# Kernel optimization log

Hardware: AMD Instinct MI355X
Metric: run time of the kernel (lower is better)

The kernel has to match this reference:

```python
import jax, jax.numpy as jnp
import numpy as np

N = 100000      # nodes per graph
E = 1600000     # edges (avg degree 16)
T = 4           # time steps
NL = 15         # num_locations
FD = 3          # feature_dim_node
H, C = 2, 6     # heads, per-head channels (hidden_channels=12)
HC = H * C


def setup_inputs():
    key = jax.random.key(0)
    ks = jax.random.split(key, 24)
    inp = {
        'node_types': jax.random.randint(ks[0], (T, N), 0, 4, dtype=jnp.int32),
        'requests': jax.random.normal(ks[1], (T, N), jnp.float32),
        'time_index': jax.random.uniform(ks[2], (T, N), dtype=jnp.float32),
        'edge_index': jax.random.randint(ks[3], (T, 2, E), 0, N, dtype=jnp.int32),
        'emb': 0.1 * jax.random.normal(ks[4], (4, FD), jnp.float32),
    }
    dims = [FD + 2, HC, HC, HC]
    k = 5
    for i, din in enumerate(dims):
        inp[f'W{i}'] = jax.random.normal(ks[k], (din, HC), jnp.float32) / np.sqrt(din); k += 1
        inp[f'as{i}'] = 0.1 * jax.random.normal(ks[k], (H, C), jnp.float32); k += 1
        inp[f'ad{i}'] = 0.1 * jax.random.normal(ks[k], (H, C), jnp.float32); k += 1
        inp[f'b{i}'] = jnp.zeros((HC,), jnp.float32); k += 1
    return inp


def gat_layer(x, src, dst, W, a_s, a_d, b):
    # PyG GATConv: linear -> per-head additive attention -> softmax over incoming
    # edges (self-loops already appended to src/dst) -> weighted aggregation.
    h = (x @ W).reshape(N, H, C)
    e_s = (h * a_s).sum(-1)                                  # [N, H]
    e_d = (h * a_d).sum(-1)                                  # [N, H]
    logits = jax.nn.leaky_relu(e_s[src] + e_d[dst], 0.2)      # [E', H]
    m = jax.ops.segment_max(logits, dst, num_segments=N)
    m = jnp.where(jnp.isfinite(m), m, 0.0)
    p = jnp.exp(logits - m[dst])
    denom = jax.ops.segment_sum(p, dst, num_segments=N)
    alpha = p / (denom[dst] + 1e-16)
    out = jax.ops.segment_sum(alpha[:, :, None] * h[src], dst, num_segments=N)
    return out.reshape(N, HC) + b


def _forward(node_types, requests, time_index, edge_index, emb, params):
    def step(nt, req, ti, ei):
        x_emb = emb[nt]                                       # [N, FD]
        tail = req[NL:]
        mean = tail.mean()
        std = tail.std(ddof=1)                                # torch.std is unbiased
        req_f = jnp.concatenate([req[:NL], (tail - mean) / std])
        x = jnp.concatenate([x_emb, req_f[:, None], ti[:, None]], axis=-1)  # [N, FD+2]
        loops = jnp.arange(N, dtype=ei.dtype)
        src = jnp.concatenate([ei[0], loops])
        dst = jnp.concatenate([ei[1], loops])
        for i in range(3):                                     # att + 2 hidden_atts
            x = jax.nn.relu(gat_layer(x, src, dst, *params[i]))
        return gat_layer(x, src, dst, *params[3])              # final_att, no act
    return jax.vmap(step)(node_types, requests, time_index, edge_index)


def reference(node_types, requests, time_index, edge_index, emb,
              W0, as0, ad0, b0, W1, as1, ad1, b1,
              W2, as2, ad2, b2, W3, as3, ad3, b3):
    params = [(W0, as0, ad0, b0), (W1, as1, ad1, b1),
              (W2, as2, ad2, b2), (W3, as3, ad3, b3)]
    return _forward(node_types, requests, time_index, edge_index, emb, params)
```

## Files before the change

### kernel.cpp

```cpp
#include <hip/hip_runtime.h>
#include <hip/hip_fp16.h>
#include <math.h>

#define NN 100000
#define EE 1600000
#define TT 4
#define NLQ 15
#define FDQ 3
#define HCQ 12
#define CAP 48
#define RECU 8
#define NCB32 ((NN + 31) / 32)
#define BKT 512
#define NBKT ((NN + BKT - 1) / BKT)
#define BCAP 9216
#define EB 4096
#define NBE ((EE + EB - 1) / EB)
#define SPB 64

typedef int v4i __attribute__((ext_vector_type(4)));
typedef unsigned v4u __attribute__((ext_vector_type(4)));

__device__ __forceinline__ unsigned pack2(float a, float b) {
    __half2 h = __floats2half2_rn(a, b);
    return *reinterpret_cast<unsigned*>(&h);
}
__device__ __forceinline__ float2 unpack2(unsigned u) {
    __half2 h = *reinterpret_cast<__half2*>(&u);
    return __half22float2(h);
}

__global__ void statsA(const float* __restrict__ req, float* __restrict__ part) {
    int t = blockIdx.y, b = blockIdx.x;
    const float* r = req + (size_t)t * NN;
    const int NP = NN - NLQ;
    __shared__ float ssum[256], ssq[256];
    float s = 0.f, q = 0.f;
    for (int i = b * 256 + threadIdx.x; i < NP; i += SPB * 256) {
        float v = r[NLQ + i]; s += v; q += v * v;
    }
    ssum[threadIdx.x] = s; ssq[threadIdx.x] = q;
    __syncthreads();
    for (int off = 128; off > 0; off >>= 1) {
        if ((int)threadIdx.x < off) {
            ssum[threadIdx.x] += ssum[threadIdx.x + off];
            ssq[threadIdx.x]  += ssq[threadIdx.x + off];
        }
        __syncthreads();
    }
    if (threadIdx.x == 0) {
        part[(t * SPB + b) * 2]     = ssum[0];
        part[(t * SPB + b) * 2 + 1] = ssq[0];
    }
}

__global__ void statsB(const float* __restrict__ part, float* __restrict__ stats) {
    int t = blockIdx.x, k = threadIdx.x;
    __shared__ float ssum[64], ssq[64];
    ssum[k] = part[(t * SPB + k) * 2];
    ssq[k]  = part[(t * SPB + k) * 2 + 1];
    __syncthreads();
    for (int off = 32; off > 0; off >>= 1) {
        if (k < off) { ssum[k] += ssum[k + off]; ssq[k] += ssq[k + off]; }
        __syncthreads();
    }
    if (k == 0) {
        float n = (float)(NN - NLQ);
        float mean = ssum[0] / n;
        float var  = (ssq[0] - ssum[0] * mean) / (n - 1.0f);
        stats[t * 2]     = mean;
        stats[t * 2 + 1] = 1.0f / sqrtf(var);
    }
}

__global__ void scatF(const int* __restrict__ ei, int* __restrict__ gcnt,
                      unsigned* __restrict__ bke) {
    int t = blockIdx.y, b = blockIdx.x;
    __shared__ unsigned sorted[EB];
    __shared__ unsigned char bid[EB];
    __shared__ int cnt_[NBKT], cur[NBKT], goff[NBKT];
    __shared__ int sv[256];
    int k = threadIdx.x;
    for (int i = k; i < NBKT; i += 256) cnt_[i] = 0;
    __syncthreads();
    int base = b * EB;
    int nvalid = (EE - base < EB) ? (EE - base) : EB;
    int n4 = nvalid >> 2;
    const v4i* dst4p = (const v4i*)(ei + (size_t)t * 2 * EE + EE + base);
    const v4i* src4p = (const v4i*)(ei + (size_t)t * 2 * EE + base);
    v4i dc[4];
#pragma unroll
    for (int j = 0; j < 4; j++) {
        int i4 = j * 256 + k;
        dc[j] = (i4 < n4) ? dst4p[i4] : (v4i)(-1);
    }
#pragma unroll
    for (int j = 0; j < 4; j++)
#pragma unroll
        for (int m = 0; m < 4; m++) {
            int d = dc[j][m];
            if (d >= 0) atomicAdd(&cnt_[d >> 9], 1);
        }
    __syncthreads();
    int v = (k < NBKT) ? cnt_[k] : 0;
    sv[k] = v;
    __syncthreads();
    for (int off = 1; off < 256; off <<= 1) {
        int x = (k >= off) ? sv[k - off] : 0;
        __syncthreads();
        sv[k] += x;
        __syncthreads();
    }
    if (k < NBKT) {
        int ex = sv[k] - v;
        cur[k]  = ex;
        int gb = atomicAdd(&gcnt[t * NBKT + k], v);
        goff[k] = k * BCAP + gb - ex;
    }
    __syncthreads();
#pragma unroll
    for (int j = 0; j < 4; j++) {
        int i4 = j * 256 + k;
        if (i4 < n4) {
            v4i s4 = src4p[i4];
#pragma unroll
            for (int m = 0; m < 4; m++) {
                int d = dc[j][m];
                int bk = d >> 9;
                int lp = atomicAdd(&cur[bk], 1);
                sorted[lp] = ((unsigned)(d & 511) << 17) | (unsigned)s4[m];
                bid[lp] = (unsigned char)bk;
            }
        }
    }
    __syncthreads();
    const size_t tb = (size_t)t * NBKT * BCAP;
    for (int p = k; p < nvalid; p += 256) {
        int B = bid[p];
        bke[tb + goff[B] + p] = sorted[p];
    }
}

__global__ void fillv2(const unsigned* __restrict__ bke, const int* __restrict__ gcnt,
                       int* __restrict__ cnt, int* __restrict__ csr) {
    extern __shared__ int sm[];
    int* cl    = sm;
    int* slots = sm + BKT;
    int t = blockIdx.y, b = blockIdx.x;
    int nbase = b * BKT;
    int nn = (NN - nbase < BKT) ? (NN - nbase) : BKT;
    for (int i = threadIdx.x; i < nn; i += 256) {
        cl[i] = 1;
        slots[i * CAP] = nbase + i;
    }
    __syncthreads();
    int nE  = gcnt[t * NBKT + b];
    int n4  = (nE + 3) >> 2;
    const v4u* bke4 = (const v4u*)(bke + (size_t)t * NBKT * BCAP + (size_t)b * BCAP);
    for (int i4 = threadIdx.x; i4 < n4; i4 += 512) {
        v4u pa = bke4[i4];
        int ib = i4 + 256;
        v4u pb = (ib < n4) ? bke4[ib] : (v4u)(0u);
        int ba = i4 << 2;
#pragma unroll
        for (int j = 0; j < 4; j++) {
            if (ba + j < nE) {
                unsigned p = pa[j];
                int dl = p >> 17, src = (int)(p & 0x1FFFF);
                int pos = atomicAdd(&cl[dl], 1);
                slots[dl * CAP + pos] = src;
            }
        }
        int bb = ib << 2;
#pragma unroll
        for (int j = 0; j < 4; j++) {
            if (bb + j < nE) {
                unsigned p = pb[j];
                int dl = p >> 17, src = (int)(p & 0x1FFFF);
                int pos = atomicAdd(&cl[dl], 1);
                slots[dl * CAP + pos] = src;
            }
        }
    }
    __syncthreads();
    const v4i* sl4 = (const v4i*)slots;
    v4i* dst4 = (v4i*)(csr + ((size_t)t * NN + nbase) * CAP);
    for (int i = threadIdx.x; i < nn * 8; i += 256) {
        int node = i >> 3, w = i & 7;
        dst4[node * 12 + w] = sl4[node * 12 + w];
    }
    for (int i = threadIdx.x; i < nn; i += 256) {
        if (cl[i] > 32) {
#pragma unroll
            for (int w = 8; w < 12; w++)
                dst4[i * 12 + w] = sl4[i * 12 + w];
        }
    }
    for (int i = threadIdx.x; i < nn; i += 256)
        cnt[t * NN + nbase + i] = cl[i];
}

__global__ void node0_kernel(const int* __restrict__ nt, const float* __restrict__ req,
                             const float* __restrict__ ti, const float* __restrict__ emb,
                             const float* __restrict__ W, const float* __restrict__ as_,
                             const float* __restrict__ ad_, const float* __restrict__ stats,
                             unsigned* __restrict__ hrec, float* __restrict__ ed) {
    __shared__ float sW[5 * HCQ], sas[HCQ], sad[HCQ];
    if (threadIdx.x < 5 * HCQ) sW[threadIdx.x] = W[threadIdx.x];
    if (threadIdx.x < HCQ) { sas[threadIdx.x] = as_[threadIdx.x]; sad[threadIdx.x] = ad_[threadIdx.x]; }
    __syncthreads();
    int id = blockIdx.x * blockDim.x + threadIdx.x;
    if (id >= TT * NN) return;
    int t = id / NN, n = id - t * NN;
    float mean = stats[t * 2], rstd = stats[t * 2 + 1];
    int typ = nt[id];
    float x[5];
    x[0] = emb[typ * FDQ + 0];
    x[1] = emb[typ * FDQ + 1];
    x[2] = emb[typ * FDQ + 2];
    float rv = req[id];
    x[3] = (n < NLQ) ? rv : (rv - mean) * rstd;
    x[4] = ti[id];
    float hv[HCQ];
#pragma unroll
    for (int c = 0; c < HCQ; c++) {
        float a = 0.f;
#pragma unroll
        for (int k = 0; k < 5; k++) a += x[k] * sW[k * HCQ + c];
        hv[c] = a;
    }
    float e0 = 0.f, e1 = 0.f, f0 = 0.f, f1 = 0.f;
#pragma unroll
    for (int c = 0; c < 6; c++) {
        e0 += hv[c] * sas[c];     f0 += hv[c] * sad[c];
        e1 += hv[6 + c] * sas[6 + c]; f1 += hv[6 + c] * sad[6 + c];
    }
    uint4* rp = (uint4*)(hrec + (size_t)id * RECU);
    rp[0] = make_uint4(pack2(hv[0], hv[1]), pack2(hv[2], hv[3]), pack2(hv[4], hv[5]), pack2(hv[6], hv[7]));
    rp[1] = make_uint4(pack2(hv[8], hv[9]), pack2(hv[10], hv[11]), __float_as_uint(e0), __float_as_uint(e1));
    ((float2*)ed)[id] = make_float2(f0, f1);
}

__global__ void edge_kernel(const int* __restrict__ cnt, const int* __restrict__ csr_src,
                            const unsigned* __restrict__ hrecI, const float* __restrict__ edI,
                            const float* __restrict__ bias,
                            const float* __restrict__ Wn, const float* __restrict__ asn,
                            const float* __restrict__ adn,
                            unsigned* __restrict__ hrecO, float* __restrict__ edO,
                            float* __restrict__ outF, int mode) {
    __shared__ float sb[HCQ], sW[HCQ * HCQ], sas[HCQ], sad[HCQ];
    if (threadIdx.x < HCQ) sb[threadIdx.x] = bias[threadIdx.x];
    if (mode == 0) {
        if (threadIdx.x < HCQ * HCQ) sW[threadIdx.x] = Wn[threadIdx.x];
        if (threadIdx.x < HCQ) { sas[threadIdx.x] = asn[threadIdx.x]; sad[threadIdx.x] = adn[threadIdx.x]; }
    }
    __syncthreads();
    int b = blockIdx.x;
    int t = b & 3;
    int nl = threadIdx.x >> 3, q = threadIdx.x & 7;
    int n = (b >> 2) * 32 + nl;
    if (n >= NN) return;
    int id = t * NN + n;
    int deg = cnt[id];
    const int*      srcs = csr_src + (size_t)id * CAP;
    const unsigned* hb   = hrecI + (size_t)t * NN * RECU;
    float2 edv = ((const float2*)edI)[id];
    float ed0 = edv.x, ed1 = edv.y;
    float d0 = 0.f, d1 = 0.f;
    float acc[HCQ];
#pragma unroll
    for (int c = 0; c < HCQ; c++) acc[c] = 0.f;

    auto process = [&](int4 s4, int ebase) {
        int rem = deg - ebase;
        int ss[4];
        ss[0] = s4.x; ss[1] = s4.y; ss[2] = s4.z; ss[3] = s4.w;
        uint4 ra[4], rb[4];
#pragma unroll
        for (int k = 0; k < 4; k++) {
            ra[k] = make_uint4(0u, 0u, 0u, 0u);
            rb[k] = make_uint4(0u, 0u, 0xFF800000u, 0xFF800000u);
        }
#pragma unroll
        for (int k = 0; k < 4; k++) {
            if (rem > k) {
                const uint4* hp = (const uint4*)(hb + (size_t)ss[k] * RECU);
                ra[k] = hp[0];
                rb[k] = hp[1];
            }
        }
#pragma unroll
        for (int k = 0; k < 4; k++) {
            float l0 = __uint_as_float(rb[k].z) + ed0; l0 = fmaxf(l0, 0.2f * l0);
            float l1 = __uint_as_float(rb[k].w) + ed1; l1 = fmaxf(l1, 0.2f * l1);
            float w0 = __expf(l0), w1 = __expf(l1);
            d0 += w0; d1 += w1;
            float2 h01 = unpack2(ra[k].x), h23 = unpack2(ra[k].y), h45 = unpack2(ra[k].z);
            float2 h67 = unpack2(ra[k].w), h89 = unpack2(rb[k].x), hab = unpack2(rb[k].y);
            acc[0] += w0 * h01.x;  acc[1] += w0 * h01.y;
            acc[2] += w0 * h23.x;  acc[3] += w0 * h23.y;
            acc[4] += w0 * h45.x;  acc[5] += w0 * h45.y;
            acc[6] += w1 * h67.x;  acc[7] += w1 * h67.y;
            acc[8]  += w1 * h89.x; acc[9]  += w1 * h89.y;
            acc[10] += w1 * hab.x; acc[11] += w1 * hab.y;
        }
    };

    int e0s = q * 4;
    if (e0s < deg) {
        int4 sA = *(const int4*)(srcs + e0s);
        process(sA, e0s);
    }
    if (q < 4) {
        int e2 = 32 + q * 4;
        if (e2 < deg) {
            int4 sC = *(const int4*)(srcs + e2);
            process(sC, e2);
        }
    }

#pragma unroll
    for (int m = 1; m <= 4; m <<= 1) {
        d0 += __shfl_xor(d0, m);
        d1 += __shfl_xor(d1, m);
#pragma unroll
        for (int c = 0; c < HCQ; c++) acc[c] += __shfl_xor(acc[c], m);
    }

    float inv0 = 1.0f / (d0 + 1e-16f);
    float inv1 = 1.0f / (d1 + 1e-16f);
    float ov[HCQ];
#pragma unroll
    for (int c = 0; c < HCQ; c++)
        ov[c] = acc[c] * ((c < 6) ? inv0 : inv1) + sb[c];

    if (mode == 1) {
        if (q < 3) {
            float4* op = (float4*)(outF + (size_t)id * HCQ);
            op[q] = make_float4(ov[4 * q], ov[4 * q + 1], ov[4 * q + 2], ov[4 * q + 3]);
        }
        return;
    }
#pragma unroll
    for (int c = 0; c < HCQ; c++) ov[c] = fmaxf(ov[c], 0.f);
    int cc = (q < 6) ? 2 * q : 0;
    float hv0 = 0.f, hv1 = 0.f;
#pragma unroll
    for (int k = 0; k < HCQ; k++) {
        hv0 += ov[k] * sW[k * HCQ + cc];
        hv1 += ov[k] * sW[k * HCQ + cc + 1];
    }
    float pe = hv0 * sas[cc] + hv1 * sas[cc + 1];
    float pf = hv0 * sad[cc] + hv1 * sad[cc + 1];
    if (q >= 6) { pe = 0.f; pf = 0.f; }
    float e0h = __shfl(pe, 0, 8) + __shfl(pe, 1, 8) + __shfl(pe, 2, 8);
    float e1h = __shfl(pe, 3, 8) + __shfl(pe, 4, 8) + __shfl(pe, 5, 8);
    float f0h = __shfl(pf, 0, 8) + __shfl(pf, 1, 8) + __shfl(pf, 2, 8);
    float f1h = __shfl(pf, 3, 8) + __shfl(pf, 4, 8) + __shfl(pf, 5, 8);
    unsigned word;
    if (q < 6)      word = pack2(hv0, hv1);
    else if (q == 6) word = __float_as_uint(e0h);
    else             word = __float_as_uint(e1h);
    hrecO[(size_t)id * RECU + q] = word;
    if (q == 0) ((float2*)edO)[id] = make_float2(f0h, f1h);
}

extern "C" void kernel_launch(void* const* d_in, const int* in_sizes, int n_in,
                              void* d_out, int out_size, void* d_ws, size_t ws_size,
                              hipStream_t stream) {
    const int*   nt  = (const int*)d_in[0];
    const float* req = (const float*)d_in[1];
    const float* ti  = (const float*)d_in[2];
    const int*   ei  = (const int*)d_in[3];
    const float* emb = (const float*)d_in[4];
    const float* W[4], *as_[4], *ad_[4], *bb[4];
    for (int l = 0; l < 4; l++) {
        W[l]   = (const float*)d_in[5 + l * 4 + 0];
        as_[l] = (const float*)d_in[5 + l * 4 + 1];
        ad_[l] = (const float*)d_in[5 + l * 4 + 2];
        bb[l]  = (const float*)d_in[5 + l * 4 + 3];
    }

    char* p = (char*)d_ws;
    auto alloc = [&](size_t bytes) -> void* {
        void* r = (void*)p;
        p += (bytes + 255) & ~(size_t)255;
        return r;
    };
    float*    stats = (float*)alloc((size_t)TT * 2 * 4);
    float*    part  = (float*)alloc((size_t)TT * SPB * 2 * 4);
    int*      cnt   = (int*)  alloc((size_t)TT * NN * 4);
    unsigned* hrecA = (unsigned*)alloc((size_t)TT * NN * RECU * 4);
    float*    edA   = (float*)alloc((size_t)TT * NN * 2 * 4);
    int*      gcnt  = (int*)  alloc((size_t)TT * NBKT * 4);
    char*     ub    = (char*)alloc((size_t)TT * NBKT * BCAP * 4);
    unsigned* bke   = (unsigned*)ub;
    unsigned* hrecB = (unsigned*)ub;
    float*    edB   = (float*)(ub + (size_t)TT * NN * RECU * 4);
    int*      csr   = (int*)  alloc((size_t)TT * NN * CAP * 4);

    hipMemsetAsync(gcnt, 0, (size_t)TT * NBKT * 4, stream);

    statsA<<<dim3(SPB, TT), 256, 0, stream>>>(req, part);
    statsB<<<TT, 64, 0, stream>>>(part, stats);

    scatF<<<dim3(NBE, TT), 256, 0, stream>>>(ei, gcnt, bke);
    size_t fillLds = (size_t)(BKT + BKT * CAP) * 4;
    fillv2<<<dim3(NBKT, TT), 256, fillLds, stream>>>(bke, gcnt, cnt, csr);

    int ngrid = (TT * NN + 255) / 256;
    int egrid2 = 4 * NCB32;
    node0_kernel<<<ngrid, 256, 0, stream>>>(nt, req, ti, emb, W[0], as_[0], ad_[0], stats, hrecA, edA);
    edge_kernel<<<egrid2, 256, 0, stream>>>(cnt, csr, hrecA, edA, bb[0], W[1], as_[1], ad_[1],
                                            hrecB, edB, nullptr, 0);
    edge_kernel<<<egrid2, 256, 0, stream>>>(cnt, csr, hrecB, edB, bb[1], W[2], as_[2], ad_[2],
                                            hrecA, edA, nullptr, 0);
    edge_kernel<<<egrid2, 256, 0, stream>>>(cnt, csr, hrecA, edA, bb[2], W[3], as_[3], ad_[3],
                                            hrecB, edB, nullptr, 0);
    edge_kernel<<<egrid2, 256, 0, stream>>>(cnt, csr, hrecB, edB, bb[3], nullptr, nullptr, nullptr,
                                            nullptr, nullptr, (float*)d_out, 1);
}
```

Before: 402.4 us.

## Halve bucket size and scatter edges directly to global buckets without LDS staging

Bucket width drops from 512 to 256 nodes, so there are more buckets, each with a smaller capacity, and fillv2 gets smaller per-block LDS and more blocks. scatF now runs 512 threads, loads src and dst together, and drops the LDS sort, prefix scan and staged copy. Each edge is written straight to global memory at a slot claimed with a shared-memory atomic cursor. This removes several syncs and the LDS staging, but the global writes become scattered rather than grouped by bucket, which may hurt write coalescing.

```diff
diff --git a/kernel.cpp b/kernel.cpp
--- a/kernel.cpp
+++ b/kernel.cpp
@@ -11,9 +11,9 @@
 #define CAP 48
 #define RECU 8
 #define NCB32 ((NN + 31) / 32)
-#define BKT 512
+#define BKT 256
 #define NBKT ((NN + BKT - 1) / BKT)
-#define BCAP 9216
+#define BCAP 4608
 #define EB 4096
 #define NBE ((EE + EB - 1) / EB)
 #define SPB 64
@@ -73,72 +73,51 @@
     }
 }
 
-__global__ void scatF(const int* __restrict__ ei, int* __restrict__ gcnt,
-                      unsigned* __restrict__ bke) {
+__global__ void __launch_bounds__(512) scatF(const int* __restrict__ ei, int* __restrict__ gcnt,
+                                             unsigned* __restrict__ bke) {
     int t = blockIdx.y, b = blockIdx.x;
-    __shared__ unsigned sorted[EB];
-    __shared__ unsigned char bid[EB];
-    __shared__ int cnt_[NBKT], cur[NBKT], goff[NBKT];
-    __shared__ int sv[256];
+    __shared__ int cnt_[NBKT], cur[NBKT];
     int k = threadIdx.x;
-    for (int i = k; i < NBKT; i += 256) cnt_[i] = 0;
+    for (int i = k; i < NBKT; i += 512) cnt_[i] = 0;
     __syncthreads();
     int base = b * EB;
     int nvalid = (EE - base < EB) ? (EE - base) : EB;
     int n4 = nvalid >> 2;
     const v4i* dst4p = (const v4i*)(ei + (size_t)t * 2 * EE + EE + base);
     const v4i* src4p = (const v4i*)(ei + (size_t)t * 2 * EE + base);
-    v4i dc[4];
-#pragma unroll
-    for (int j = 0; j < 4; j++) {
-        int i4 = j * 256 + k;
-        dc[j] = (i4 < n4) ? dst4p[i4] : (v4i)(-1);
-    }
-#pragma unroll
-    for (int j = 0; j < 4; j++)
+    v4i dc[2], sc[2];
+#pragma unroll
+    for (int j = 0; j < 2; j++) {
+        int i4 = j * 512 + k;
+        bool v = i4 < n4;
+        dc[j] = v ? dst4p[i4] : (v4i)(-1);
+        sc[j] = v ? src4p[i4] : (v4i)(0);
+    }
+#pragma unroll
+    for (int j = 0; j < 2; j++)
 #pragma unroll
         for (int m = 0; m < 4; m++) {
             int d = dc[j][m];
-            if (d >= 0) atomicAdd(&cnt_[d >> 9], 1);
-        }
-    __syncthreads();
-    int v = (k < NBKT) ? cnt_[k] : 0;
-    sv[k] = v;
-    __syncthreads();
-    for (int off = 1; off < 256; off <<= 1) {
-        int x = (k >= off) ? sv[k - off] : 0;
-        __syncthreads();
-        sv[k] += x;
-        __syncthreads();
-    }
-    if (k < NBKT) {
-        int ex = sv[k] - v;
-        cur[k]  = ex;
-        int gb = atomicAdd(&gcnt[t * NBKT + k], v);
-        goff[k] = k * BCAP + gb - ex;
-    }
-    __syncthreads();
-#pragma unroll
-    for (int j = 0; j < 4; j++) {
-        int i4 = j * 256 + k;
-        if (i4 < n4) {
-            v4i s4 = src4p[i4];
-#pragma unroll
-            for (int m = 0; m < 4; m++) {
-                int d = dc[j][m];
-                int bk = d >> 9;
-                int lp = atomicAdd(&cur[bk], 1);
-                sorted[lp] = ((unsigned)(d & 511) << 17) | (unsigned)s4[m];
-                bid[lp] = (unsigned char)bk;
+            if (d >= 0) atomicAdd(&cnt_[d >> 8], 1);
+        }
+    __syncthreads();
+    for (int i = k; i < NBKT; i += 512) {
+        int v = cnt_[i];
+        int gb = (v > 0) ? atomicAdd(&gcnt[t * NBKT + i], v) : 0;
+        cur[i] = i * BCAP + gb;
+    }
+    __syncthreads();
+    const size_t tb = (size_t)t * NBKT * BCAP;
+#pragma unroll
+    for (int j = 0; j < 2; j++)
+#pragma unroll
+        for (int m = 0; m < 4; m++) {
+            int d = dc[j][m];
+            if (d >= 0) {
+                int lp = atomicAdd(&cur[d >> 8], 1);
+                bke[tb + lp] = ((unsigned)(d & 255) << 17) | (unsigned)sc[j][m];
             }
         }
-    }
-    __syncthreads();
-    const size_t tb = (size_t)t * NBKT * BCAP;
-    for (int p = k; p < nvalid; p += 256) {
-        int B = bid[p];
-        bke[tb + goff[B] + p] = sorted[p];
-    }
 }
 
 __global__ void fillv2(const unsigned* __restrict__ bke, const int* __restrict__ gcnt,
@@ -404,7 +383,7 @@
     statsA<<<dim3(SPB, TT), 256, 0, stream>>>(req, part);
     statsB<<<TT, 64, 0, stream>>>(part, stats);
 
-    scatF<<<dim3(NBE, TT), 256, 0, stream>>>(ei, gcnt, bke);
+    scatF<<<dim3(NBE, TT), 512, 0, stream>>>(ei, gcnt, bke);
     size_t fillLds = (size_t)(BKT + BKT * CAP) * 4;
     fillv2<<<dim3(NBKT, TT), 256, fillLds, stream>>>(bke, gcnt, cnt, csr);
 
```

After: 406.7 us. No clear change (+1.1%).
